# Optimization experiments

Hardware: AMD Instinct MI355X
Metric: run time of the kernel (lower is better)

The kernel has to match this reference:

```python
import jax, jax.numpy as jnp
import numpy as np

M_TOKENS, D_IN, D_OUT = 4096, 4096, 16384


def setup_inputs() -> dict:
    key = jax.random.key(0)
    k1, k2, k3, k4 = jax.random.split(key, 4)
    x = jax.random.normal(k1, (M_TOKENS, D_IN), dtype=jnp.float32)
    # pre-quantized int8 weight, stored [K, N] as in qweight_kn
    qweight_kn = jax.random.randint(k2, (D_IN, D_OUT), -127, 128, dtype=jnp.int8)
    # per-output-channel weight dequant scales (float16 buffer, used as fp32 in kernel)
    weight_scales = jax.random.uniform(k3, (D_OUT,), dtype=jnp.float32, minval=1e-3, maxval=2e-2)
    bias = jax.random.normal(k4, (D_OUT,), dtype=jnp.float32) * 0.01
    return {"x": x, "qweight_kn": qweight_kn, "weight_scales": weight_scales, "bias": bias}


def reference(x, qweight_kn, weight_scales, bias):
    target_dtype = x.dtype
    x2 = x.reshape(-1, x.shape[-1])  # [M, K]
    # dynamic per-token (per-row) symmetric quantization
    x_max = jnp.max(jnp.abs(x2), axis=-1, keepdims=True).astype(jnp.float32) + 1e-5
    x_scales = x_max / 127.0  # [M, 1]
    x_int8 = jnp.clip(jnp.round(x2.astype(jnp.float32) / x_scales), -128, 127).astype(jnp.int8)
    acc = jax.lax.dot_general(
        x_int8, qweight_kn,
        dimension_numbers=(((1,), (0,)), ((), ())),
        preferred_element_type=jnp.int32,
    )  # [M, N] int32
    # fused dequant: row act-scale * col weight-scale, plus bias
    c = acc.astype(jnp.float32) * x_scales * weight_scales[None, :].astype(jnp.float32)
    c = c + bias[None, :]
    out = c.astype(jnp.bfloat16)  # kernel stores bf16
    return out.reshape(*x.shape[:-1], -1).astype(target_dtype)
```

## Files before the change

### kernel.cpp

```cpp
#include <hip/hip_runtime.h>
#include <hip/hip_bf16.h>
#include <stdint.h>

typedef int v4i __attribute__((ext_vector_type(4)));
typedef int v16i __attribute__((ext_vector_type(16)));

#define GM 4096
#define GN 16384
#define GK 4096
#define BM 256
#define BN 256
#define BK 128
#define NTILES (GK / BK)

__device__ __forceinline__ void gload16(const void* g, void* l) {
  __builtin_amdgcn_global_load_lds(
      (const __attribute__((address_space(1))) void*)g,
      (__attribute__((address_space(3))) void*)l, 16, 0, 0);
}

__global__ __launch_bounds__(256) void quant_rows(
    const float* __restrict__ x, int8_t* __restrict__ xq,
    float* __restrict__ xs, int K) {
  const int row = blockIdx.x;
  const int t = threadIdx.x;
  const float4* src = (const float4*)(x + (size_t)row * K) + t * 4;
  float4 v[4];
  float m = 0.f;
#pragma unroll
  for (int i = 0; i < 4; ++i) {
    v[i] = src[i];
    m = fmaxf(m, fmaxf(fmaxf(fabsf(v[i].x), fabsf(v[i].y)),
                       fmaxf(fabsf(v[i].z), fabsf(v[i].w))));
  }
#pragma unroll
  for (int off = 1; off < 64; off <<= 1)
    m = fmaxf(m, __shfl_xor(m, off, 64));
  __shared__ float wmax[4];
  if ((t & 63) == 0) wmax[t >> 6] = m;
  __syncthreads();
  const float gm = fmaxf(fmaxf(wmax[0], wmax[1]), fmaxf(wmax[2], wmax[3]));
  const float scale = (gm + 1e-5f) / 127.0f;
  if (t == 0) xs[row] = scale;
  unsigned packed[4];
#pragma unroll
  for (int i = 0; i < 4; ++i) {
    float fv[4] = {v[i].x, v[i].y, v[i].z, v[i].w};
    unsigned p = 0;
#pragma unroll
    for (int j = 0; j < 4; ++j) {
      int q = (int)rintf(fv[j] / scale);
      q = max(-128, min(127, q));
      p |= (unsigned)(q & 0xff) << (8 * j);
    }
    packed[i] = p;
  }
  *(int4*)(xq + (size_t)row * K + t * 16) =
      make_int4((int)packed[0], (int)packed[1], (int)packed[2], (int)packed[3]);
}

__global__ __launch_bounds__(256) void transpose_pack(
    const int* __restrict__ W32, int8_t* __restrict__ Wt, int K, int N) {
  __shared__ __align__(16) int8_t tile[64][80];
  const int t = threadIdx.x;
  const int n0 = blockIdx.x * 64;
  const int k0 = blockIdx.y * 64;
  const int ln = t & 63;
  const int wv = t >> 6;
#pragma unroll
  for (int it = 0; it < 16; ++it) {
    const int kk = wv * 16 + it;
    tile[ln][kk] = (int8_t)W32[(size_t)(k0 + kk) * N + n0 + ln];
  }
  __syncthreads();
  const int kb = wv * 16;
  const int4 v = *(const int4*)&tile[ln][kb];
  *(int4*)(Wt + (size_t)(n0 + ln) * K + k0 + kb) = v;
}

__global__ __launch_bounds__(512, 2) void gemm_i8(
    const int8_t* __restrict__ Xq, const int8_t* __restrict__ Wt,
    const float* __restrict__ xs, const float* __restrict__ wsc,
    const float* __restrict__ bias, float* __restrict__ C) {
  __shared__ __align__(16) int8_t lA[2][BM][BK];
  __shared__ __align__(16) int8_t lB[2][BN][BK];

  const int t = threadIdx.x;
  const int lane = t & 63;
  const int w = t >> 6;
  const int wr = w >> 2;
  const int wc = w & 3;
  const int l31 = lane & 31;
  const int kg2 = lane >> 5;

  const int bid = blockIdx.x;
  const int xcd = bid & 7;
  const int q = bid >> 3;
  const int tm = q & 15;
  const int tn = xcd * 8 + (q >> 4);
  const size_t rowA0 = (size_t)tm * BM;
  const size_t rowB0 = (size_t)tn * BN;

  const int8_t* XqB = Xq + rowA0 * GK;
  const int8_t* WtB = Wt + rowB0 * GK;
  int srcOff[4], dstOff[4];
#pragma unroll
  for (int i = 0; i < 4; ++i) {
    const int slot0 = (i * 8 + w) * 64;
    const int slot = slot0 + lane;
    const int r = slot >> 3;
    const int c = (slot & 7) ^ (r & 7);
    srcOff[i] = r * GK + c * 16;
    dstOff[i] = slot0 * 16;
  }

#define STAGE(KT, D)                                                        \
  {                                                                         \
    const int ko = (KT)*BK;                                                 \
    _Pragma("unroll") for (int i = 0; i < 4; ++i)                           \
        gload16(XqB + srcOff[i] + ko, (int8_t*)&lA[(D)][0][0] + dstOff[i]); \
    _Pragma("unroll") for (int i = 0; i < 4; ++i)                           \
        gload16(WtB + srcOff[i] + ko, (int8_t*)&lB[(D)][0][0] + dstOff[i]); \
  }

  int ck[4];
#pragma unroll
  for (int s = 0; s < 4; ++s) ck[s] = ((2 * s + kg2) ^ (l31 & 7)) * 16;

  v16i acc[4][2] = {};
  v4i areg[4][4], breg[2][4];

#define RD_A(MI, D)                                                 \
  {                                                                 \
    const int8_t* p = &lA[(D)][wr * 128 + (MI)*32 + l31][0];        \
    _Pragma("unroll") for (int s = 0; s < 4; ++s)                   \
        areg[MI][s] = *(const v4i*)(p + ck[s]);                     \
  }
#define RD_B(NJ, D)                                                 \
  {                                                                 \
    const int8_t* p = &lB[(D)][wc * 64 + (NJ)*32 + l31][0];         \
    _Pragma("unroll") for (int s = 0; s < 4; ++s)                   \
        breg[NJ][s] = *(const v4i*)(p + ck[s]);                     \
  }

#define MFMA_F(MI, NJ)                                                        \
  _Pragma("unroll") for (int s = 0; s < 4; ++s)                               \
      acc[MI][NJ] = __builtin_amdgcn_mfma_i32_32x32x32_i8(                    \
          areg[MI][s], breg[NJ][s], acc[MI][NJ], 0, 0, 0);

  STAGE(0, 0);

  for (int kt = 0; kt < NTILES; ++kt) {
    const int d = kt & 1;
    asm volatile("s_waitcnt vmcnt(0)" ::: "memory");
    __builtin_amdgcn_s_barrier();
    if (kt + 1 < NTILES) STAGE(kt + 1, d ^ 1);
    RD_A(0, d);
    RD_A(1, d);
    RD_B(0, d);
    __builtin_amdgcn_sched_barrier(0);
    RD_B(1, d);
    __builtin_amdgcn_sched_barrier(0);
    RD_A(2, d);
    RD_A(3, d);
    __builtin_amdgcn_sched_barrier(0);
    asm volatile("s_waitcnt lgkmcnt(12)" ::: "memory");
    __builtin_amdgcn_sched_barrier(0);
    __builtin_amdgcn_s_setprio(1);
    MFMA_F(0, 0);
    MFMA_F(1, 0);
    __builtin_amdgcn_s_setprio(0);
    asm volatile("s_waitcnt lgkmcnt(8)" ::: "memory");
    __builtin_amdgcn_sched_barrier(0);
    __builtin_amdgcn_s_setprio(1);
    MFMA_F(0, 1);
    MFMA_F(1, 1);
    __builtin_amdgcn_s_setprio(0);
    asm volatile("s_waitcnt lgkmcnt(0)" ::: "memory");
    __builtin_amdgcn_sched_barrier(0);
    __builtin_amdgcn_s_setprio(1);
    MFMA_F(2, 0);
    MFMA_F(3, 0);
    MFMA_F(2, 1);
    MFMA_F(3, 1);
    __builtin_amdgcn_s_setprio(0);
  }

#pragma unroll
  for (int nj = 0; nj < 2; ++nj) {
    const int col_l = wc * 64 + nj * 32 + l31;
    const float wsv = wsc[rowB0 + col_l];
    const float bv = bias[rowB0 + col_l];
#pragma unroll
    for (int mi = 0; mi < 4; ++mi) {
#pragma unroll
      for (int r = 0; r < 16; ++r) {
        const size_t row =
            rowA0 + wr * 128 + mi * 32 + (r & 3) + 8 * (r >> 2) + 4 * kg2;
        const float f = (float)acc[mi][nj][r] * xs[row] * wsv + bv;
        C[row * GN + rowB0 + col_l] = __bfloat162float(__float2bfloat16(f));
      }
    }
  }
}

extern "C" void kernel_launch(void* const* d_in, const int* in_sizes, int n_in,
                              void* d_out, int out_size, void* d_ws, size_t ws_size,
                              hipStream_t stream) {
  const int M = GM, K = GK, N = GN;
  const float* x = (const float*)d_in[0];
  const int* W32 = (const int*)d_in[1];
  const float* wsc = (const float*)d_in[2];
  const float* bias = (const float*)d_in[3];
  float* out = (float*)d_out;

  float* xs = (float*)d_ws;
  int8_t* Xq = (int8_t*)d_ws + 16384;
  int8_t* Wt = (int8_t*)d_ws + 16384 + (size_t)M * K;

  transpose_pack<<<dim3(N / 64, K / 64), 256, 0, stream>>>(W32, Wt, K, N);
  quant_rows<<<M, 256, 0, stream>>>(x, Xq, xs, K);
  gemm_i8<<<dim3((M / BM) * (N / BN)), 512, 0, stream>>>(Xq, Wt, xs, wsc, bias,
                                                         out);
}
```

Measured before the change: 486.7 us.

## Pre-pack weights into MFMA fragment order and load B directly to registers

The transpose kernel now writes the int8 weight into a layout that matches the MFMA operand fragments for each 256-column tile, K-step and 32-column subtile. The GEMM drops the LDS buffer for B and has each wave read its B fragments straight from global memory into registers, while A is still staged through LDS. The wave grid changes from 2x4 to 4x2 so each wave covers 64 rows by 128 columns. This cuts LDS capacity and LDS read traffic for B, but B is no longer shared through LDS, so global/L2 traffic per block goes up. The last iteration also issues an extra, unused A stage because the tile index wraps.

```diff
diff --git a/kernel.cpp b/kernel.cpp
--- a/kernel.cpp
+++ b/kernel.cpp
@@ -60,7 +60,7 @@
 }
 
 __global__ __launch_bounds__(256) void transpose_pack(
-    const int* __restrict__ W32, int8_t* __restrict__ Wt, int K, int N) {
+    const int* __restrict__ W32, int8_t* __restrict__ Wt2, int K, int N) {
   __shared__ __align__(16) int8_t tile[64][80];
   const int t = threadIdx.x;
   const int n0 = blockIdx.x * 64;
@@ -73,23 +73,27 @@
     tile[ln][kk] = (int8_t)W32[(size_t)(k0 + kk) * N + n0 + ln];
   }
   __syncthreads();
-  const int kb = wv * 16;
-  const int4 v = *(const int4*)&tile[ln][kb];
-  *(int4*)(Wt + (size_t)(n0 + ln) * K + k0 + kb) = v;
+  const int f2 = wv >> 1, s2 = wv & 1;
+  const int4 v = *(const int4*)&tile[f2 * 32 + (ln & 31)][s2 * 32 + (ln >> 5) * 16];
+  const int tn = n0 >> 8;
+  const int fb = ((n0 & 255) >> 5) + f2;
+  const int kt = k0 >> 7;
+  const int sb = ((k0 & 127) >> 5) + s2;
+  *(int4*)(Wt2 +
+           ((((size_t)(tn * 32 + kt) * 8 + fb) * 4 + sb) * 64 + ln) * 16) = v;
 }
 
 __global__ __launch_bounds__(512, 2) void gemm_i8(
-    const int8_t* __restrict__ Xq, const int8_t* __restrict__ Wt,
+    const int8_t* __restrict__ Xq, const int8_t* __restrict__ Wt2,
     const float* __restrict__ xs, const float* __restrict__ wsc,
     const float* __restrict__ bias, float* __restrict__ C) {
   __shared__ __align__(16) int8_t lA[2][BM][BK];
-  __shared__ __align__(16) int8_t lB[2][BN][BK];
 
   const int t = threadIdx.x;
   const int lane = t & 63;
   const int w = t >> 6;
-  const int wr = w >> 2;
-  const int wc = w & 3;
+  const int wr = w >> 1;
+  const int wc = w & 1;
   const int l31 = lane & 31;
   const int kg2 = lane >> 5;
 
@@ -102,7 +106,6 @@
   const size_t rowB0 = (size_t)tn * BN;
 
   const int8_t* XqB = Xq + rowA0 * GK;
-  const int8_t* WtB = Wt + rowB0 * GK;
   int srcOff[4], dstOff[4];
 #pragma unroll
   for (int i = 0; i < 4; ++i) {
@@ -115,37 +118,32 @@
   }
 
 #define STAGE(KT, D)                                                        \
-  {                                                                         \
-    const int ko = (KT)*BK;                                                 \
-    _Pragma("unroll") for (int i = 0; i < 4; ++i)                           \
-        gload16(XqB + srcOff[i] + ko, (int8_t*)&lA[(D)][0][0] + dstOff[i]); \
-    _Pragma("unroll") for (int i = 0; i < 4; ++i)                           \
-        gload16(WtB + srcOff[i] + ko, (int8_t*)&lB[(D)][0][0] + dstOff[i]); \
-  }
+  _Pragma("unroll") for (int i = 0; i < 4; ++i)                             \
+      gload16(XqB + srcOff[i] + (KT)*BK, (int8_t*)&lA[(D)][0][0] + dstOff[i]);
 
   int ck[4];
 #pragma unroll
   for (int s = 0; s < 4; ++s) ck[s] = ((2 * s + kg2) ^ (l31 & 7)) * 16;
 
-  v16i acc[4][2] = {};
-  v4i areg[4][4], breg[2][4];
-
-#define RD_A(MI, D)                                                 \
-  {                                                                 \
-    const int8_t* p = &lA[(D)][wr * 128 + (MI)*32 + l31][0];        \
-    _Pragma("unroll") for (int s = 0; s < 4; ++s)                   \
-        areg[MI][s] = *(const v4i*)(p + ck[s]);                     \
-  }
-#define RD_B(NJ, D)                                                 \
-  {                                                                 \
-    const int8_t* p = &lB[(D)][wc * 64 + (NJ)*32 + l31][0];         \
-    _Pragma("unroll") for (int s = 0; s < 4; ++s)                   \
-        breg[NJ][s] = *(const v4i*)(p + ck[s]);                     \
-  }
-
-#define MFMA_F(MI, NJ)                                                        \
-  _Pragma("unroll") for (int s = 0; s < 4; ++s)                               \
-      acc[MI][NJ] = __builtin_amdgcn_mfma_i32_32x32x32_i8(                    \
+  v16i acc[2][4] = {};
+  v4i areg[2][4], breg[4][4];
+
+  const int8_t* bq = Wt2 + (size_t)tn * 1048576 + wc * 16384 + lane * 16;
+
+#define RD_A(MI, D)                                               \
+  {                                                               \
+    const int8_t* p = &lA[(D)][wr * 64 + (MI)*32 + l31][0];       \
+    _Pragma("unroll") for (int s = 0; s < 4; ++s)                 \
+        areg[MI][s] = *(const v4i*)(p + ck[s]);                   \
+  }
+#define LOADB(NJ, KT)                                             \
+  _Pragma("unroll") for (int s = 0; s < 4; ++s)                   \
+      breg[NJ][s] =                                               \
+          *(const v4i*)(bq + (size_t)(KT)*32768 + (NJ)*4096 + s * 1024);
+
+#define MFMA_F(MI, NJ)                                            \
+  _Pragma("unroll") for (int s = 0; s < 4; ++s)                   \
+      acc[MI][NJ] = __builtin_amdgcn_mfma_i32_32x32x32_i8(        \
           areg[MI][s], breg[NJ][s], acc[MI][NJ], 0, 0, 0);
 
   STAGE(0, 0);
@@ -154,49 +152,46 @@
     const int d = kt & 1;
     asm volatile("s_waitcnt vmcnt(0)" ::: "memory");
     __builtin_amdgcn_s_barrier();
-    if (kt + 1 < NTILES) STAGE(kt + 1, d ^ 1);
+    LOADB(0, kt);
+    LOADB(1, kt);
+    __builtin_amdgcn_sched_barrier(0);
+    LOADB(2, kt);
+    LOADB(3, kt);
+    __builtin_amdgcn_sched_barrier(0);
+    STAGE((kt + 1) & (NTILES - 1), d ^ 1);
+    __builtin_amdgcn_sched_barrier(0);
     RD_A(0, d);
     RD_A(1, d);
-    RD_B(0, d);
-    __builtin_amdgcn_sched_barrier(0);
-    RD_B(1, d);
-    __builtin_amdgcn_sched_barrier(0);
-    RD_A(2, d);
-    RD_A(3, d);
-    __builtin_amdgcn_sched_barrier(0);
-    asm volatile("s_waitcnt lgkmcnt(12)" ::: "memory");
+    __builtin_amdgcn_sched_barrier(0);
+    asm volatile("s_waitcnt vmcnt(12) lgkmcnt(0)" ::: "memory");
     __builtin_amdgcn_sched_barrier(0);
     __builtin_amdgcn_s_setprio(1);
     MFMA_F(0, 0);
     MFMA_F(1, 0);
-    __builtin_amdgcn_s_setprio(0);
-    asm volatile("s_waitcnt lgkmcnt(8)" ::: "memory");
-    __builtin_amdgcn_sched_barrier(0);
-    __builtin_amdgcn_s_setprio(1);
     MFMA_F(0, 1);
     MFMA_F(1, 1);
     __builtin_amdgcn_s_setprio(0);
-    asm volatile("s_waitcnt lgkmcnt(0)" ::: "memory");
+    asm volatile("s_waitcnt vmcnt(4)" ::: "memory");
     __builtin_amdgcn_sched_barrier(0);
     __builtin_amdgcn_s_setprio(1);
-    MFMA_F(2, 0);
-    MFMA_F(3, 0);
-    MFMA_F(2, 1);
-    MFMA_F(3, 1);
+    MFMA_F(0, 2);
+    MFMA_F(1, 2);
+    MFMA_F(0, 3);
+    MFMA_F(1, 3);
     __builtin_amdgcn_s_setprio(0);
   }
 
 #pragma unroll
-  for (int nj = 0; nj < 2; ++nj) {
-    const int col_l = wc * 64 + nj * 32 + l31;
+  for (int nj = 0; nj < 4; ++nj) {
+    const int col_l = wc * 128 + nj * 32 + l31;
     const float wsv = wsc[rowB0 + col_l];
     const float bv = bias[rowB0 + col_l];
 #pragma unroll
-    for (int mi = 0; mi < 4; ++mi) {
+    for (int mi = 0; mi < 2; ++mi) {
 #pragma unroll
       for (int r = 0; r < 16; ++r) {
         const size_t row =
-            rowA0 + wr * 128 + mi * 32 + (r & 3) + 8 * (r >> 2) + 4 * kg2;
+            rowA0 + wr * 64 + mi * 32 + (r & 3) + 8 * (r >> 2) + 4 * kg2;
         const float f = (float)acc[mi][nj][r] * xs[row] * wsv + bv;
         C[row * GN + rowB0 + col_l] = __bfloat162float(__float2bfloat16(f));
       }
@@ -216,10 +211,10 @@
 
   float* xs = (float*)d_ws;
   int8_t* Xq = (int8_t*)d_ws + 16384;
-  int8_t* Wt = (int8_t*)d_ws + 16384 + (size_t)M * K;
-
-  transpose_pack<<<dim3(N / 64, K / 64), 256, 0, stream>>>(W32, Wt, K, N);
+  int8_t* Wt2 = (int8_t*)d_ws + 16384 + (size_t)M * K;
+
+  transpose_pack<<<dim3(N / 64, K / 64), 256, 0, stream>>>(W32, Wt2, K, N);
   quant_rows<<<M, 256, 0, stream>>>(x, Xq, xs, K);
-  gemm_i8<<<dim3((M / BM) * (N / BN)), 512, 0, stream>>>(Xq, Wt, xs, wsc, bias,
+  gemm_i8<<<dim3((M / BM) * (N / BN)), 512, 0, stream>>>(Xq, Wt2, xs, wsc, bias,
                                                          out);
 }
```

Result: slower. 511.0 us (+5.0%).

## Software-pipeline LDS fragment reads across k-tiles in int8 GEMM main loop

Applied to the files above, without the earlier changes.

Restructures the GEMM main loop so the first A/B fragment reads for the next k-tile are issued right after the barrier, ahead of the last MFMA group of the current tile. The loop is unrolled by two with a TILE_BODY macro. Each tile's global-to-LDS stage is now issued two tiles ahead into the buffer just drained, after its barrier. LDS read waits are interleaved with MFMA groups (lgkmcnt 4/8/0) to hide LDS latency behind matrix ops. The aim is to shrink the MFMA idle bubble at each tile boundary. The cost is more intricate wait-count and register-reuse bookkeeping.

```diff
diff --git a/kernel.cpp b/kernel.cpp
--- a/kernel.cpp
+++ b/kernel.cpp
@@ -130,60 +130,84 @@
   v16i acc[4][2] = {};
   v4i areg[4][4], breg[2][4];
 
-#define RD_A(MI, D)                                                 \
-  {                                                                 \
-    const int8_t* p = &lA[(D)][wr * 128 + (MI)*32 + l31][0];        \
-    _Pragma("unroll") for (int s = 0; s < 4; ++s)                   \
-        areg[MI][s] = *(const v4i*)(p + ck[s]);                     \
-  }
-#define RD_B(NJ, D)                                                 \
-  {                                                                 \
-    const int8_t* p = &lB[(D)][wc * 64 + (NJ)*32 + l31][0];         \
-    _Pragma("unroll") for (int s = 0; s < 4; ++s)                   \
-        breg[NJ][s] = *(const v4i*)(p + ck[s]);                     \
-  }
-
-#define MFMA_F(MI, NJ)                                                        \
-  _Pragma("unroll") for (int s = 0; s < 4; ++s)                               \
-      acc[MI][NJ] = __builtin_amdgcn_mfma_i32_32x32x32_i8(                    \
+#define RD_A(MI, D)                                               \
+  {                                                               \
+    const int8_t* p = &lA[(D)][wr * 128 + (MI)*32 + l31][0];      \
+    _Pragma("unroll") for (int s = 0; s < 4; ++s)                 \
+        areg[MI][s] = *(const v4i*)(p + ck[s]);                   \
+  }
+#define RD_B(NJ, D)                                               \
+  {                                                               \
+    const int8_t* p = &lB[(D)][wc * 64 + (NJ)*32 + l31][0];       \
+    _Pragma("unroll") for (int s = 0; s < 4; ++s)                 \
+        breg[NJ][s] = *(const v4i*)(p + ck[s]);                   \
+  }
+
+#define MFMA_F(MI, NJ)                                            \
+  _Pragma("unroll") for (int s = 0; s < 4; ++s)                   \
+      acc[MI][NJ] = __builtin_amdgcn_mfma_i32_32x32x32_i8(        \
           areg[MI][s], breg[NJ][s], acc[MI][NJ], 0, 0, 0);
 
+#define SB __builtin_amdgcn_sched_barrier(0)
+
+#define TILE_BODY(KT, D)                                                     \
+  {                                                                          \
+           \
+    RD_B(1, D);                                                              \
+    SB;                                                                      \
+    asm volatile("s_waitcnt lgkmcnt(4)" ::: "memory");                       \
+    SB;                                                                      \
+    __builtin_amdgcn_s_setprio(1);                                           \
+    MFMA_F(0, 0);                                                            \
+    MFMA_F(1, 0);                                                            \
+    __builtin_amdgcn_s_setprio(0);                                           \
+          \
+    RD_A(2, D);                                                              \
+    RD_A(3, D);                                                              \
+    SB;                                                                      \
+    asm volatile("s_waitcnt lgkmcnt(8)" ::: "memory");                       \
+    SB;                                                                      \
+    __builtin_amdgcn_s_setprio(1);                                           \
+    MFMA_F(0, 1);                                                            \
+    MFMA_F(1, 1);                                                            \
+    __builtin_amdgcn_s_setprio(0);                                           \
+                    \
+    asm volatile("s_waitcnt lgkmcnt(0)" ::: "memory");                       \
+    SB;                                                                      \
+    __builtin_amdgcn_s_setprio(1);                                           \
+    MFMA_F(2, 0);                                                            \
+    MFMA_F(3, 0);                                                            \
+    __builtin_amdgcn_s_setprio(0);                                           \
+                        \
+    asm volatile("s_waitcnt vmcnt(0)" ::: "memory");                         \
+    __builtin_amdgcn_s_barrier();                                            \
+    SB;                                                                      \
+    if ((KT) + 2 < NTILES) STAGE((KT) + 2, D);                               \
+    SB;                                                                      \
+    if ((KT) + 1 < NTILES) {                                                 \
+      RD_A(0, (D) ^ 1);                                                      \
+      RD_A(1, (D) ^ 1);                                                      \
+      RD_B(0, (D) ^ 1);                                                      \
+    }                                                                        \
+    SB;                                                                      \
+    __builtin_amdgcn_s_setprio(1);                                           \
+    MFMA_F(2, 1);                                                            \
+    MFMA_F(3, 1);                                                            \
+    __builtin_amdgcn_s_setprio(0);                                           \
+  }
+
   STAGE(0, 0);
-
-  for (int kt = 0; kt < NTILES; ++kt) {
-    const int d = kt & 1;
-    asm volatile("s_waitcnt vmcnt(0)" ::: "memory");
-    __builtin_amdgcn_s_barrier();
-    if (kt + 1 < NTILES) STAGE(kt + 1, d ^ 1);
-    RD_A(0, d);
-    RD_A(1, d);
-    RD_B(0, d);
-    __builtin_amdgcn_sched_barrier(0);
-    RD_B(1, d);
-    __builtin_amdgcn_sched_barrier(0);
-    RD_A(2, d);
-    RD_A(3, d);
-    __builtin_amdgcn_sched_barrier(0);
-    asm volatile("s_waitcnt lgkmcnt(12)" ::: "memory");
-    __builtin_amdgcn_sched_barrier(0);
-    __builtin_amdgcn_s_setprio(1);
-    MFMA_F(0, 0);
-    MFMA_F(1, 0);
-    __builtin_amdgcn_s_setprio(0);
-    asm volatile("s_waitcnt lgkmcnt(8)" ::: "memory");
-    __builtin_amdgcn_sched_barrier(0);
-    __builtin_amdgcn_s_setprio(1);
-    MFMA_F(0, 1);
-    MFMA_F(1, 1);
-    __builtin_amdgcn_s_setprio(0);
-    asm volatile("s_waitcnt lgkmcnt(0)" ::: "memory");
-    __builtin_amdgcn_sched_barrier(0);
-    __builtin_amdgcn_s_setprio(1);
-    MFMA_F(2, 0);
-    MFMA_F(3, 0);
-    MFMA_F(2, 1);
-    MFMA_F(3, 1);
-    __builtin_amdgcn_s_setprio(0);
+  asm volatile("s_waitcnt vmcnt(0)" ::: "memory");
+  __builtin_amdgcn_s_barrier();
+  STAGE(1, 1);
+  RD_A(0, 0);
+  RD_A(1, 0);
+  RD_B(0, 0);
+  SB;
+
+  for (int kt = 0; kt < NTILES; kt += 2) {
+    TILE_BODY(kt, 0);
+    TILE_BODY(kt + 1, 1);
   }
 
 #pragma unroll
```

New measurement: 722.1 us. +48.4%, slower.
